# Performance work log

Measured on AMD Instinct MI355X. Metric: run time of the kernel, lower is better.

The kernel has to match this reference:

```python
import jax, jax.numpy as jnp
import numpy as np

HIDDEN = 1024
HEADS = 16
HEAD_DIM = HIDDEN // HEADS  # 64
MAX_SEQ = 2048


def _rope_tables():
    # RotaryEmbedding buffers: freqs_cos/sin of shape [max_seq_len, head_dim//2]
    inv_freq = 1.0 / (10000.0 ** (jnp.arange(0, HEAD_DIM, 2, dtype=jnp.float32) / HEAD_DIM))
    t = jnp.arange(MAX_SEQ, dtype=jnp.float32)
    freqs = t[:, None] * inv_freq[None, :]
    return jnp.cos(freqs), jnp.sin(freqs)


def setup_inputs() -> dict:
    key = jax.random.key(0)
    k1, k2, k3 = jax.random.split(key, 3)
    x = jax.random.normal(k1, (2, 2048, HIDDEN), dtype=jnp.float32)
    qkv_w = jax.random.normal(k2, (HIDDEN, 3 * HIDDEN), dtype=jnp.float32) * 0.02
    qkv_b = jnp.zeros((3 * HIDDEN,), dtype=jnp.float32)
    out_w = jax.random.normal(k3, (HIDDEN, HIDDEN), dtype=jnp.float32) * 0.02
    out_b = jnp.zeros((HIDDEN,), dtype=jnp.float32)
    return {"x": x, "qkv_w": qkv_w, "qkv_b": qkv_b, "out_w": out_w, "out_b": out_b}


def reference(x, qkv_w, qkv_b, out_w, out_b):
    b, s, _ = x.shape
    qkv = x @ qkv_w + qkv_b                                   # [b, s, 3*hidden]
    qkv = qkv.reshape(b, s, HEADS, 3 * HEAD_DIM).transpose(0, 2, 1, 3)  # [b, h, s, 3*hd]
    q, k, v = jnp.split(qkv, 3, axis=-1)                      # each [b, h, s, hd]

    # Faithful to source quirk: rotary() is called on [b, h, s, hd] tensors so
    # x.shape[1] == num_heads -> seq_pos = arange(num_heads); tables are indexed
    # by HEAD index and broadcast over the sequence axis.
    cos_tab, sin_tab = _rope_tables()
    cos = cos_tab[:HEADS][None, :, None, :]                   # [1, h, 1, hd/2]
    sin = sin_tab[:HEADS][None, :, None, :]

    def rot(u):
        u1 = u[..., : HEAD_DIM // 2]
        u2 = u[..., HEAD_DIM // 2 :]
        return jnp.concatenate([u1 * cos - u2 * sin, u2 * cos + u1 * sin], axis=-1)

    q = rot(q)
    k = rot(k)

    scores = jnp.einsum("bhqd,bhkd->bhqk", q, k) / (HEAD_DIM ** 0.5)  # [b, h, s, s]
    attn = jax.nn.softmax(scores.astype(jnp.float32), axis=-1).astype(scores.dtype)
    out = jnp.einsum("bhqk,bhkd->bhqd", attn, v)              # [b, h, s, hd]
    out = out.transpose(0, 2, 1, 3).reshape(b, s, HEADS * HEAD_DIM)
    return out @ out_w + out_b
```

## Files before the change

kernel.cpp:

```cpp
#include <hip/hip_runtime.h>
#include <hip/hip_bf16.h>
#include <cstdint>
#include <cstddef>

typedef float  f32x4  __attribute__((ext_vector_type(4)));
typedef __bf16 bf16x8 __attribute__((ext_vector_type(8)));
typedef __bf16 bf16x4 __attribute__((ext_vector_type(4)));

#define HIDDEN 1024
#define SEQ    2048
#define BATCH  2
#define NQKV   3072
#define MTOT   4096

__device__ __forceinline__ __bf16 f2bf(float f) {
  unsigned u = __builtin_bit_cast(unsigned, f);
  u += 0x7FFFu + ((u >> 16) & 1u);
  unsigned short s = (unsigned short)(u >> 16);
  return __builtin_bit_cast(__bf16, s);
}

__device__ __forceinline__ unsigned pk2(float a, float b) {
  unsigned ua = __builtin_bit_cast(unsigned, a) + 0x8000u;
  unsigned ub = __builtin_bit_cast(unsigned, b) + 0x8000u;
  return __builtin_amdgcn_perm(ub, ua, 0x07060302u);
}

__device__ __forceinline__ float fexp2(float x) {
#if __has_builtin(__builtin_amdgcn_exp2f)
  return __builtin_amdgcn_exp2f(x);
#else
  return exp2f(x);
#endif
}

__device__ __forceinline__ void async16(const void* g, void* l) {
  __builtin_amdgcn_global_load_lds((__attribute__((address_space(1))) void*)(g),
                                   (__attribute__((address_space(3))) void*)(l),
                                   16, 0, 0);
}

#define MFMA16(a, b, c) __builtin_amdgcn_mfma_f32_16x16x32_bf16((a), (b), (c), 0, 0, 0)

__global__ __launch_bounds__(256) void k_prep(const float* __restrict__ x,
                                              __bf16* __restrict__ xb,
                                              const float* __restrict__ qkv_w,
                                              __bf16* __restrict__ wqkT,
                                              const float* __restrict__ out_w,
                                              __bf16* __restrict__ woT) {
  __shared__ float tile[64][65];
  const int bid = blockIdx.x, t = threadIdx.x;
  if (bid < 4096) {
    int i = bid * 256 + t;
    float4 v = ((const float4*)x)[i];
    bf16x4 o;
    o[0] = f2bf(v.x); o[1] = f2bf(v.y); o[2] = f2bf(v.z); o[3] = f2bf(v.w);
    ((bf16x4*)xb)[i] = o;
    return;
  }
  const float* W; __bf16* WT; int N, bx, by;
  if (bid < 4864) { int g = bid - 4096; W = qkv_w; WT = wqkT; N = NQKV;  bx = g % 48; by = g / 48; }
  else            { int g = bid - 4864; W = out_w; WT = woT;  N = HIDDEN; bx = g % 16; by = g / 16; }
  const int K = HIDDEN;
  int tx = t & 63, ty = t >> 6;
  int n0 = bx * 64, k0 = by * 64;
#pragma unroll
  for (int r = 0; r < 16; r++) {
    int row = r * 4 + ty;
    tile[row][tx] = W[(size_t)(k0 + row) * N + n0 + tx];
  }
  __syncthreads();
#pragma unroll
  for (int i2 = 0; i2 < 2; i2++) {
    int cc = i2 * 256 + t;
    int n = cc >> 3, ch = cc & 7;
    bf16x8 o;
#pragma unroll
    for (int j = 0; j < 8; j++) o[j] = f2bf(tile[ch * 8 + j][n]);
    *(bf16x8*)(WT + (size_t)(n0 + n) * K + k0 + ch * 8) = o;
  }
}

__global__ __launch_bounds__(512, 2) void k_qkv(const __bf16* __restrict__ A,
                                                const __bf16* __restrict__ BT,
                                                const float* __restrict__ bias,
                                                __bf16* __restrict__ Cout,
                                                __bf16* __restrict__ vt) {
  const int K = HIDDEN;
  __shared__ __align__(16) __bf16 As[2][2][8192];
  __shared__ __align__(16) __bf16 Bs[2][12288];
  const int t = threadIdx.x;
  const int lane = t & 63, wv = t >> 6;
  const int ln = lane & 15, quad = lane >> 4;
  const int wm = (wv >> 2) * 128, wn = (wv & 3) * 48;

  const int lin = blockIdx.x;
  const int xcd = lin & 7, wi = lin >> 3;
  const int bxi = (xcd & 3) * 4 + (wi & 3);
  const int byi = (xcd >> 2) * 8 + (wi >> 2);
  const int m0 = byi * 256, n0 = bxi * 192;

  auto stA = [&](int kt, int h) {
    __bf16* dst = &As[kt & 1][h][0];
    const __bf16* src = A + (size_t)m0 * K + kt * 64;
#pragma unroll
    for (int i = 0; i < 2; i++) {
      int tt = i * 512 + t;
      int sr = tt >> 3, ch = tt & 7;
      int gr = (sr & 63) + ((sr >> 6) << 7) + h * 64;
      async16(src + (size_t)gr * K + ((ch ^ (sr & 7)) * 8), dst + tt * 8);
    }
  };
  auto stB = [&](int kt) {
    __bf16* dst = &Bs[kt & 1][0];
    const __bf16* src = BT + (size_t)n0 * K + kt * 64;
#pragma unroll
    for (int i = 0; i < 3; i++) {
      int tt = i * 512 + t;
      int row = tt >> 3, ch = tt & 7;
      async16(src + (size_t)row * K + ((ch ^ (row & 7)) * 8), dst + tt * 8);
    }
  };

  const f32x4 zero4 = {0.f, 0.f, 0.f, 0.f};
  f32x4 acc[8][3];
#pragma unroll
  for (int i = 0; i < 8; i++)
#pragma unroll
    for (int j = 0; j < 3; j++) acc[i][j] = zero4;

  stA(0, 0); stB(0); stA(0, 1); stA(1, 0); stB(1);

  bf16x8 a0[4], a1[4], b0[3], b1[3];
  const int sra = ln + ((wv >> 2) << 6);
  const int srb = (wv & 3) * 48 + ln;
  const int swz = ln & 7;

  const int NT = K / 64;
  for (int kt = 0; kt < NT; kt++) {
    const int p = kt & 1;
    if (kt < NT - 1) asm volatile("s_waitcnt vmcnt(5)" ::: "memory");
    else             asm volatile("s_waitcnt vmcnt(0)" ::: "memory");
    __builtin_amdgcn_s_barrier();
    const __bf16* A0 = &As[p][0][0];
    const __bf16* A1 = &As[p][1][0];
    const __bf16* Bb = &Bs[p][0];
    {
#pragma unroll
      for (int m = 0; m < 4; m++)
        a0[m] = *(const bf16x8*)(A0 + (sra + m * 16) * 64 + ((quad ^ swz) * 8));
#pragma unroll
      for (int n = 0; n < 3; n++)
        b0[n] = *(const bf16x8*)(Bb + (srb + n * 16) * 64 + ((quad ^ swz) * 8));
      if (kt + 1 < NT) stA(kt + 1, 1);
      __builtin_amdgcn_s_barrier();
      asm volatile("s_waitcnt lgkmcnt(0)" ::: "memory");
      __builtin_amdgcn_sched_barrier(0);
      __builtin_amdgcn_s_setprio(1);
#pragma unroll
      for (int m = 0; m < 4; m++)
#pragma unroll
        for (int n = 0; n < 3; n++)
          acc[m][n] = MFMA16(a0[m], b0[n], acc[m][n]);
      __builtin_amdgcn_s_setprio(0);
      __builtin_amdgcn_s_barrier();
    }
    {
#pragma unroll
      for (int m = 0; m < 4; m++)
        a1[m] = *(const bf16x8*)(A0 + (sra + m * 16) * 64 + (((4 + quad) ^ swz) * 8));
#pragma unroll
      for (int n = 0; n < 3; n++)
        b1[n] = *(const bf16x8*)(Bb + (srb + n * 16) * 64 + (((4 + quad) ^ swz) * 8));
      __builtin_amdgcn_s_barrier();
      asm volatile("s_waitcnt lgkmcnt(0)" ::: "memory");
      __builtin_amdgcn_sched_barrier(0);
      __builtin_amdgcn_s_setprio(1);
#pragma unroll
      for (int m = 0; m < 4; m++)
#pragma unroll
        for (int n = 0; n < 3; n++)
          acc[m][n] = MFMA16(a1[m], b1[n], acc[m][n]);
      __builtin_amdgcn_s_setprio(0);
      __builtin_amdgcn_s_barrier();
    }
    {
#pragma unroll
      for (int m = 0; m < 4; m++)
        a0[m] = *(const bf16x8*)(A1 + (sra + m * 16) * 64 + ((quad ^ swz) * 8));
      if (kt + 2 < NT) stA(kt + 2, 0);
      __builtin_amdgcn_s_barrier();
      asm volatile("s_waitcnt lgkmcnt(0)" ::: "memory");
      __builtin_amdgcn_sched_barrier(0);
      __builtin_amdgcn_s_setprio(1);
#pragma unroll
      for (int m = 0; m < 4; m++)
#pragma unroll
        for (int n = 0; n < 3; n++)
          acc[4 + m][n] = MFMA16(a0[m], b0[n], acc[4 + m][n]);
      __builtin_amdgcn_s_setprio(0);
      __builtin_amdgcn_s_barrier();
    }
    {
#pragma unroll
      for (int m = 0; m < 4; m++)
        a1[m] = *(const bf16x8*)(A1 + (sra + m * 16) * 64 + (((4 + quad) ^ swz) * 8));
      if (kt + 2 < NT) stB(kt + 2);
      __builtin_amdgcn_s_barrier();
      asm volatile("s_waitcnt lgkmcnt(0)" ::: "memory");
      __builtin_amdgcn_sched_barrier(0);
      __builtin_amdgcn_s_setprio(1);
#pragma unroll
      for (int m = 0; m < 4; m++)
#pragma unroll
        for (int n = 0; n < 3; n++)
          acc[4 + m][n] = MFMA16(a1[m], b1[n], acc[4 + m][n]);
      __builtin_amdgcn_s_setprio(0);
    }
  }

  const float CE = 0.125f * 1.44269504089f;
#pragma unroll
  for (int nt = 0; nt < 3; nt++) {
    int g = n0 + wn + nt * 16;
    int col = g + ln;
    float bv = bias[col];
    int off = g % 192;
    if (off < 128) {
      float scl = (off < 64) ? CE : 1.0f;
#pragma unroll
      for (int mt = 0; mt < 8; mt++) {
#pragma unroll
        for (int r = 0; r < 4; r++) {
          int row = m0 + wm + mt * 16 + quad * 4 + r;
          Cout[(size_t)row * NQKV + col] = f2bf((acc[mt][nt][r] + bv) * scl);
        }
      }
    } else {
      int hg = g / 192;
      int d  = off - 128 + ln;
#pragma unroll
      for (int mt = 0; mt < 8; mt++) {
        int rowb = m0 + wm + mt * 16;
        int bb = rowb >> 11;
        int s  = rowb & 2047;
        int sblk = s >> 7;
        int blk  = (s >> 4) & 7;
        int pp = (blk & 3) * 32 + quad * 8 + ((blk >> 2) << 2);
        uint2 o;
        o.x = pk2(acc[mt][nt][0] + bv, acc[mt][nt][1] + bv);
        o.y = pk2(acc[mt][nt][2] + bv, acc[mt][nt][3] + bv);
        *(uint2*)(vt + ((size_t)((bb * 16 + hg) * 64 + d)) * SEQ + sblk * 128 + pp) = o;
      }
    }
  }
}

__global__ __launch_bounds__(512, 2) void k_out(const __bf16* __restrict__ A,
                                                const __bf16* __restrict__ BT,
                                                const float* __restrict__ bias,
                                                float* __restrict__ Cout) {
  const int K = HIDDEN, N = HIDDEN;
  __shared__ __align__(16) __bf16 As[2][2][4096];
  __shared__ __align__(16) __bf16 Bs[2][8192];
  const int t = threadIdx.x;
  const int lane = t & 63, wv = t >> 6;
  const int ln = lane & 15, quad = lane >> 4;
  const int wm = (wv >> 2) * 64, wn = (wv & 3) * 32;

  const int lin = blockIdx.x;
  const int xcd = lin & 7, wi = lin >> 3;
  const int bxi = (xcd & 1) * 4 + (wi & 3);
  const int byi = (xcd >> 1) * 8 + (wi >> 2);
  const int m0 = byi * 128, n0 = bxi * 128;

  auto stA = [&](int kt, int h) {
    __bf16* dst = &As[kt & 1][h][0];
    const __bf16* src = A + (size_t)m0 * K + kt * 64;
    int sr = t >> 3, ch = t & 7;
    int gr = (sr & 31) + ((sr >> 5) << 6) + h * 32;
    async16(src + (size_t)gr * K + ((ch ^ (sr & 7)) * 8), dst + t * 8);
  };
  auto stB = [&](int kt) {
    __bf16* dst = &Bs[kt & 1][0];
    const __bf16* src = BT + (size_t)n0 * K + kt * 64;
#pragma unroll
    for (int i = 0; i < 2; i++) {
      int tt = i * 512 + t;
      int row = tt >> 3, ch = tt & 7;
      async16(src + (size_t)row * K + ((ch ^ (row & 7)) * 8), dst + tt * 8);
    }
  };

  const f32x4 zero4 = {0.f, 0.f, 0.f, 0.f};
  f32x4 acc[4][2];
#pragma unroll
  for (int i = 0; i < 4; i++)
#pragma unroll
    for (int j = 0; j < 2; j++) acc[i][j] = zero4;

  stA(0, 0); stB(0); stA(0, 1); stA(1, 0); stB(1);

  bf16x8 af[2][2], bfr[2][2];
  const int sra = ln + ((wv >> 2) << 5);
  const int srb = wn + ln;
  const int swz = ln & 7;

  const int NT = K / 64;
  for (int kt = 0; kt < NT; kt++) {
    const int p = kt & 1;
    if (kt < NT - 1) asm volatile("s_waitcnt vmcnt(3)" ::: "memory");
    else             asm volatile("s_waitcnt vmcnt(0)" ::: "memory");
    __builtin_amdgcn_s_barrier();
    const __bf16* A0 = &As[p][0][0];
    const __bf16* A1 = &As[p][1][0];
    const __bf16* Bb = &Bs[p][0];
    {
#pragma unroll
      for (int m = 0; m < 2; m++)
#pragma unroll
        for (int kk = 0; kk < 2; kk++)
          af[m][kk] = *(const bf16x8*)(A0 + (sra + m * 16) * 64 + (((kk * 4 + quad) ^ swz) * 8));
#pragma unroll
      for (int n = 0; n < 2; n++)
#pragma unroll
        for (int kk = 0; kk < 2; kk++)
          bfr[n][kk] = *(const bf16x8*)(Bb + (srb + n * 16) * 64 + (((kk * 4 + quad) ^ swz) * 8));
      if (kt + 1 < NT) stA(kt + 1, 1);
      __builtin_amdgcn_s_barrier();
      asm volatile("s_waitcnt lgkmcnt(0)" ::: "memory");
      __builtin_amdgcn_sched_barrier(0);
      __builtin_amdgcn_s_setprio(1);
#pragma unroll
      for (int m = 0; m < 2; m++)
#pragma unroll
        for (int n = 0; n < 2; n++) {
          acc[m][n] = MFMA16(af[m][0], bfr[n][0], acc[m][n]);
          acc[m][n] = MFMA16(af[m][1], bfr[n][1], acc[m][n]);
        }
      __builtin_amdgcn_s_setprio(0);
      __builtin_amdgcn_s_barrier();
    }
    {
#pragma unroll
      for (int m = 0; m < 2; m++)
#pragma unroll
        for (int kk = 0; kk < 2; kk++)
          af[m][kk] = *(const bf16x8*)(A1 + (sra + m * 16) * 64 + (((kk * 4 + quad) ^ swz) * 8));
      if (kt + 2 < NT) { stA(kt + 2, 0); stB(kt + 2); }
      __builtin_amdgcn_s_barrier();
      asm volatile("s_waitcnt lgkmcnt(0)" ::: "memory");
      __builtin_amdgcn_sched_barrier(0);
      __builtin_amdgcn_s_setprio(1);
#pragma unroll
      for (int m = 0; m < 2; m++)
#pragma unroll
        for (int n = 0; n < 2; n++) {
          acc[2 + m][n] = MFMA16(af[m][0], bfr[n][0], acc[2 + m][n]);
          acc[2 + m][n] = MFMA16(af[m][1], bfr[n][1], acc[2 + m][n]);
        }
      __builtin_amdgcn_s_setprio(0);
    }
  }

#pragma unroll
  for (int h = 0; h < 2; h++)
#pragma unroll
    for (int n = 0; n < 2; n++) {
      int col = n0 + wn + n * 16 + ln;
      float bv = bias[col];
#pragma unroll
      for (int m = 0; m < 2; m++)
#pragma unroll
        for (int r = 0; r < 4; r++) {
          int row = m0 + wm + h * 32 + m * 16 + quad * 4 + r;
          Cout[(size_t)row * N + col] = acc[h * 2 + m][n][r] + bv;
        }
    }
}

__global__ __launch_bounds__(512, 4) void k_attn(const __bf16* __restrict__ qkv,
                                                 const __bf16* __restrict__ vt,
                                                 __bf16* __restrict__ aout) {
  __shared__ __align__(16) __bf16 smem[32768];
  const int t = threadIdx.x;
  const int lane = t & 63, wv = t >> 6;
  const int ln = lane & 15, quad = lane >> 4;
  const int sw8 = (quad ^ ((ln >> 1) & 3)) * 8;

  int gid = blockIdx.x;
  int slot = gid & 7, j = gid >> 3;
  int bh = slot * 4 + (j >> 4);
  int qt0 = j & 15;
  const int b = bh >> 4, h = bh & 15;
  const int q0 = qt0 * 128;

  const __bf16* qbase = qkv + (size_t)b * SEQ * NQKV + h * 192;
  const __bf16* kbase = qbase + 64;
  const __bf16* vbase = vt + (size_t)bh * 64 * SEQ;

#pragma unroll
  for (int i = 0; i < 2; i++) {
    int tt = i * 512 + t;
    int hh = tt >> 9, row = (tt >> 2) & 127, ch = tt & 3;
    int chs = ch ^ ((row >> 1) & 3);
    async16(kbase + (size_t)row * NQKV + hh * 32 + chs * 8, smem + tt * 8);
  }
#pragma unroll
  for (int i = 0; i < 2; i++) {
    int tt = i * 512 + t;
    int c = tt >> 8, d = (tt >> 2) & 63, w = tt & 3;
    int ws = w ^ ((d >> 1) & 3);
    async16(vbase + (size_t)d * SEQ + c * 32 + ws * 8, smem + 16384 + tt * 8);
  }

  bf16x8 qf[2];
#pragma unroll
  for (int dc = 0; dc < 2; dc++)
    qf[dc] = *(const bf16x8*)(qbase + (size_t)(q0 + wv * 16 + ln) * NQKV + dc * 32 + quad * 8);

  union { unsigned u[4]; bf16x8 v; } ones;
  ones.u[0] = ones.u[1] = ones.u[2] = ones.u[3] = 0x3F803F80u;

  const f32x4 zero4 = {0.f, 0.f, 0.f, 0.f};
  f32x4 O[4];
  f32x4 Ol = zero4;
#pragma unroll
  for (int dt = 0; dt < 4; dt++) O[dt] = zero4;

  for (int it = 0; it < SEQ / 128; it++) {
    __syncthreads();
    const __bf16* Ks = smem + (it & 1) * 8192;
    const __bf16* Vs = smem + 16384 + (it & 1) * 8192;
    if (it + 1 < SEQ / 128) {
      __bf16* Kd = smem + ((it + 1) & 1) * 8192;
      __bf16* Vd = smem + 16384 + ((it + 1) & 1) * 8192;
      const __bf16* kn = kbase + (size_t)(it + 1) * 128 * NQKV;
      const __bf16* vn = vbase + (it + 1) * 128;
#pragma unroll
      for (int i = 0; i < 2; i++) {
        int tt = i * 512 + t;
        int hh = tt >> 9, row = (tt >> 2) & 127, ch = tt & 3;
        int chs = ch ^ ((row >> 1) & 3);
        async16(kn + (size_t)row * NQKV + hh * 32 + chs * 8, Kd + tt * 8);
      }
#pragma unroll
      for (int i = 0; i < 2; i++) {
        int tt = i * 512 + t;
        int c = tt >> 8, d = (tt >> 2) & 63, w = tt & 3;
        int ws = w ^ ((d >> 1) & 3);
        async16(vn + (size_t)d * SEQ + c * 32 + ws * 8, Vd + tt * 8);
      }
    }

    unsigned Pp[8][2];
#pragma unroll
    for (int blk = 0; blk < 8; blk++) {
      bf16x8 kf0 = *(const bf16x8*)(Ks +        (blk * 16 + ln) * 32 + sw8);
      bf16x8 kf1 = *(const bf16x8*)(Ks + 4096 + (blk * 16 + ln) * 32 + sw8);
      __builtin_amdgcn_s_setprio(1);
      f32x4 s = MFMA16(kf0, qf[0], zero4);
      s = MFMA16(kf1, qf[1], s);
      __builtin_amdgcn_s_setprio(0);
      Pp[blk][0] = pk2(fexp2(s[0]), fexp2(s[1]));
      Pp[blk][1] = pk2(fexp2(s[2]), fexp2(s[3]));
    }
#pragma unroll
    for (int kc = 0; kc < 4; kc++) {
      union { bf16x8 v; unsigned u[4]; } pf;
      pf.u[0] = Pp[kc][0]; pf.u[1] = Pp[kc][1];
      pf.u[2] = Pp[kc + 4][0]; pf.u[3] = Pp[kc + 4][1];
      __builtin_amdgcn_s_setprio(1);
      Ol = MFMA16(pf.v, ones.v, Ol);
#pragma unroll
      for (int dt = 0; dt < 4; dt++) {
        bf16x8 vf = *(const bf16x8*)(Vs + kc * 2048 + (dt * 16 + ln) * 32 + sw8);
        O[dt] = MFMA16(pf.v, vf, O[dt]);
      }
      __builtin_amdgcn_s_setprio(0);
    }
  }

  __bf16* stage = smem + wv * 1024;
#pragma unroll
  for (int r = 0; r < 4; r++) {
    float ir = 1.0f / Ol[r];
#pragma unroll
    for (int dt = 0; dt < 4; dt++)
      stage[(quad * 4 + r) * 64 + dt * 16 + ln] = f2bf(O[dt][r] * ir);
  }
  __bf16* obase = aout + (size_t)(b * SEQ + q0 + wv * 16) * HIDDEN + h * 64;
#pragma unroll
  for (int i = 0; i < 2; i++) {
    int tt = i * 64 + lane; int row = tt >> 3, ch = tt & 7;
    *(bf16x8*)(obase + (size_t)row * HIDDEN + ch * 8) = *(const bf16x8*)(stage + row * 64 + ch * 8);
  }
}

extern "C" void kernel_launch(void* const* d_in, const int* in_sizes, int n_in,
                              void* d_out, int out_size, void* d_ws, size_t ws_size,
                              hipStream_t stream) {
  const float* x     = (const float*)d_in[0];
  const float* qkv_w = (const float*)d_in[1];
  const float* qkv_b = (const float*)d_in[2];
  const float* out_w = (const float*)d_in[3];
  const float* out_b = (const float*)d_in[4];

  char* ws = (char*)d_ws;
  __bf16* xb   = (__bf16*)(ws);
  __bf16* wqkT = (__bf16*)(ws + 8388608);
  __bf16* woT  = (__bf16*)(ws + 14680064);
  __bf16* qkv  = (__bf16*)(ws + 16777216);
  __bf16* vt   = (__bf16*)(ws + 41943040);
  __bf16* aout = (__bf16*)(ws + 50331648);

  k_prep<<<5120, 256, 0, stream>>>(x, xb, qkv_w, wqkT, out_w, woT);
  k_qkv<<<256, 512, 0, stream>>>(xb, wqkT, qkv_b, qkv, vt);
  k_attn<<<512, 512, 0, stream>>>(qkv, vt, aout);
  k_out<<<256, 512, 0, stream>>>(aout, woT, out_b, (float*)d_out);
}
```

Before: 172.4 us.

## Process two query tiles per attention block to reuse K/V tiles

Each attention block now handles 256 query rows instead of 128: every wave keeps two Q fragments and two sets of output accumulators. Each K/V tile loaded into shared memory feeds twice as many MFMAs, and the grid is halved. This cuts K/V global traffic and LDS reads per unit of work, in exchange for more registers (launch bounds lowered to 2), lower occupancy and fewer blocks (256) to spread across the CUs.

```diff
diff --git a/kernel.cpp b/kernel.cpp
--- a/kernel.cpp
+++ b/kernel.cpp
@@ -379,7 +379,7 @@
     }
 }
 
-__global__ __launch_bounds__(512, 4) void k_attn(const __bf16* __restrict__ qkv,
+__global__ __launch_bounds__(512, 2) void k_attn(const __bf16* __restrict__ qkv,
                                                  const __bf16* __restrict__ vt,
                                                  __bf16* __restrict__ aout) {
   __shared__ __align__(16) __bf16 smem[32768];
@@ -390,10 +390,10 @@
 
   int gid = blockIdx.x;
   int slot = gid & 7, j = gid >> 3;
-  int bh = slot * 4 + (j >> 4);
-  int qt0 = j & 15;
+  int bh = slot * 4 + (j >> 3);
+  int qt0 = j & 7;
   const int b = bh >> 4, h = bh & 15;
-  const int q0 = qt0 * 128;
+  const int q0 = qt0 * 256;
 
   const __bf16* qbase = qkv + (size_t)b * SEQ * NQKV + h * 192;
   const __bf16* kbase = qbase + 64;
@@ -414,19 +414,24 @@
     async16(vbase + (size_t)d * SEQ + c * 32 + ws * 8, smem + 16384 + tt * 8);
   }
 
-  bf16x8 qf[2];
-#pragma unroll
-  for (int dc = 0; dc < 2; dc++)
-    qf[dc] = *(const bf16x8*)(qbase + (size_t)(q0 + wv * 16 + ln) * NQKV + dc * 32 + quad * 8);
+  bf16x8 qf[2][2];
+#pragma unroll
+  for (int u = 0; u < 2; u++)
+#pragma unroll
+    for (int dc = 0; dc < 2; dc++)
+      qf[u][dc] = *(const bf16x8*)(qbase + (size_t)(q0 + u * 128 + wv * 16 + ln) * NQKV + dc * 32 + quad * 8);
 
   union { unsigned u[4]; bf16x8 v; } ones;
   ones.u[0] = ones.u[1] = ones.u[2] = ones.u[3] = 0x3F803F80u;
 
   const f32x4 zero4 = {0.f, 0.f, 0.f, 0.f};
-  f32x4 O[4];
-  f32x4 Ol = zero4;
-#pragma unroll
-  for (int dt = 0; dt < 4; dt++) O[dt] = zero4;
+  f32x4 O[2][4];
+  f32x4 Ol[2];
+  Ol[0] = zero4; Ol[1] = zero4;
+#pragma unroll
+  for (int u = 0; u < 2; u++)
+#pragma unroll
+    for (int dt = 0; dt < 4; dt++) O[u][dt] = zero4;
 
   for (int it = 0; it < SEQ / 128; it++) {
     __syncthreads();
@@ -453,47 +458,61 @@
       }
     }
 
-    unsigned Pp[8][2];
+    unsigned Pp[2][8][2];
 #pragma unroll
     for (int blk = 0; blk < 8; blk++) {
       bf16x8 kf0 = *(const bf16x8*)(Ks +        (blk * 16 + ln) * 32 + sw8);
       bf16x8 kf1 = *(const bf16x8*)(Ks + 4096 + (blk * 16 + ln) * 32 + sw8);
       __builtin_amdgcn_s_setprio(1);
-      f32x4 s = MFMA16(kf0, qf[0], zero4);
-      s = MFMA16(kf1, qf[1], s);
-      __builtin_amdgcn_s_setprio(0);
-      Pp[blk][0] = pk2(fexp2(s[0]), fexp2(s[1]));
-      Pp[blk][1] = pk2(fexp2(s[2]), fexp2(s[3]));
+      f32x4 s0 = MFMA16(kf0, qf[0][0], zero4);
+      f32x4 s1 = MFMA16(kf0, qf[1][0], zero4);
+      s0 = MFMA16(kf1, qf[0][1], s0);
+      s1 = MFMA16(kf1, qf[1][1], s1);
+      __builtin_amdgcn_s_setprio(0);
+      Pp[0][blk][0] = pk2(fexp2(s0[0]), fexp2(s0[1]));
+      Pp[0][blk][1] = pk2(fexp2(s0[2]), fexp2(s0[3]));
+      Pp[1][blk][0] = pk2(fexp2(s1[0]), fexp2(s1[1]));
+      Pp[1][blk][1] = pk2(fexp2(s1[2]), fexp2(s1[3]));
     }
 #pragma unroll
     for (int kc = 0; kc < 4; kc++) {
-      union { bf16x8 v; unsigned u[4]; } pf;
-      pf.u[0] = Pp[kc][0]; pf.u[1] = Pp[kc][1];
-      pf.u[2] = Pp[kc + 4][0]; pf.u[3] = Pp[kc + 4][1];
-      __builtin_amdgcn_s_setprio(1);
-      Ol = MFMA16(pf.v, ones.v, Ol);
+      union { bf16x8 v; unsigned u[4]; } pf0, pf1;
+      pf0.u[0] = Pp[0][kc][0]; pf0.u[1] = Pp[0][kc][1];
+      pf0.u[2] = Pp[0][kc + 4][0]; pf0.u[3] = Pp[0][kc + 4][1];
+      pf1.u[0] = Pp[1][kc][0]; pf1.u[1] = Pp[1][kc][1];
+      pf1.u[2] = Pp[1][kc + 4][0]; pf1.u[3] = Pp[1][kc + 4][1];
+      __builtin_amdgcn_s_setprio(1);
+      Ol[0] = MFMA16(pf0.v, ones.v, Ol[0]);
+      Ol[1] = MFMA16(pf1.v, ones.v, Ol[1]);
 #pragma unroll
       for (int dt = 0; dt < 4; dt++) {
         bf16x8 vf = *(const bf16x8*)(Vs + kc * 2048 + (dt * 16 + ln) * 32 + sw8);
-        O[dt] = MFMA16(pf.v, vf, O[dt]);
+        O[0][dt] = MFMA16(pf0.v, vf, O[0][dt]);
+        O[1][dt] = MFMA16(pf1.v, vf, O[1][dt]);
       }
       __builtin_amdgcn_s_setprio(0);
     }
   }
 
-  __bf16* stage = smem + wv * 1024;
-#pragma unroll
-  for (int r = 0; r < 4; r++) {
-    float ir = 1.0f / Ol[r];
-#pragma unroll
-    for (int dt = 0; dt < 4; dt++)
-      stage[(quad * 4 + r) * 64 + dt * 16 + ln] = f2bf(O[dt][r] * ir);
-  }
-  __bf16* obase = aout + (size_t)(b * SEQ + q0 + wv * 16) * HIDDEN + h * 64;
-#pragma unroll
-  for (int i = 0; i < 2; i++) {
-    int tt = i * 64 + lane; int row = tt >> 3, ch = tt & 7;
-    *(bf16x8*)(obase + (size_t)row * HIDDEN + ch * 8) = *(const bf16x8*)(stage + row * 64 + ch * 8);
+  __bf16* stage = smem + (wv & 3) * 2048 + (wv >> 2) * 16384;
+#pragma unroll
+  for (int u = 0; u < 2; u++)
+#pragma unroll
+    for (int r = 0; r < 4; r++) {
+      float ir = 1.0f / Ol[u][r];
+#pragma unroll
+      for (int dt = 0; dt < 4; dt++)
+        stage[u * 1024 + (quad * 4 + r) * 64 + dt * 16 + ln] = f2bf(O[u][dt][r] * ir);
+    }
+#pragma unroll
+  for (int u = 0; u < 2; u++) {
+    __bf16* obase = aout + (size_t)(b * SEQ + q0 + u * 128 + wv * 16) * HIDDEN + h * 64;
+#pragma unroll
+    for (int i = 0; i < 2; i++) {
+      int tt = i * 64 + lane; int row = tt >> 3, ch = tt & 7;
+      *(bf16x8*)(obase + (size_t)row * HIDDEN + ch * 8) =
+          *(const bf16x8*)(stage + u * 1024 + row * 64 + ch * 8);
+    }
   }
 }
 
@@ -516,6 +535,6 @@
 
   k_prep<<<5120, 256, 0, stream>>>(x, xb, qkv_w, wqkT, out_w, woT);
   k_qkv<<<256, 512, 0, stream>>>(xb, wqkT, qkv_b, qkv, vt);
-  k_attn<<<512, 512, 0, stream>>>(qkv, vt, aout);
+  k_attn<<<256, 512, 0, stream>>>(qkv, vt, aout);
   k_out<<<256, 512, 0, stream>>>(aout, woT, out_b, (float*)d_out);
 }
```

Result: no change. 173.2 us (+0.5%).

## Software-pipeline attention loop: overlap next QK^T with current PV

Applied to the files above, without the earlier changes.

Restructures the attention main loop into a two-stage software pipeline. The QK^T and exp for tile it+1 are computed while the PV product for tile it runs, using two register P buffers and a manually unrolled even/odd loop. K is prefetched two tiles ahead and V one tile ahead. The goal is to interleave the exp/VALU work with MFMA and hide shared-memory load latency, at the cost of more registers (a second P buffer) and different sync placement.

```diff
diff --git a/kernel.cpp b/kernel.cpp
--- a/kernel.cpp
+++ b/kernel.cpp
@@ -399,20 +399,30 @@
   const __bf16* kbase = qbase + 64;
   const __bf16* vbase = vt + (size_t)bh * 64 * SEQ;
 
-#pragma unroll
-  for (int i = 0; i < 2; i++) {
-    int tt = i * 512 + t;
-    int hh = tt >> 9, row = (tt >> 2) & 127, ch = tt & 3;
-    int chs = ch ^ ((row >> 1) & 3);
-    async16(kbase + (size_t)row * NQKV + hh * 32 + chs * 8, smem + tt * 8);
-  }
-#pragma unroll
-  for (int i = 0; i < 2; i++) {
-    int tt = i * 512 + t;
-    int c = tt >> 8, d = (tt >> 2) & 63, w = tt & 3;
-    int ws = w ^ ((d >> 1) & 3);
-    async16(vbase + (size_t)d * SEQ + c * 32 + ws * 8, smem + 16384 + tt * 8);
-  }
+  auto stageK = [&](int it) {
+    __bf16* Kd = smem + (it & 1) * 8192;
+    const __bf16* kn = kbase + (size_t)it * 128 * NQKV;
+#pragma unroll
+    for (int i = 0; i < 2; i++) {
+      int tt = i * 512 + t;
+      int hh = tt >> 9, row = (tt >> 2) & 127, ch = tt & 3;
+      int chs = ch ^ ((row >> 1) & 3);
+      async16(kn + (size_t)row * NQKV + hh * 32 + chs * 8, Kd + tt * 8);
+    }
+  };
+  auto stageV = [&](int it) {
+    __bf16* Vd = smem + 16384 + (it & 1) * 8192;
+    const __bf16* vn = vbase + it * 128;
+#pragma unroll
+    for (int i = 0; i < 2; i++) {
+      int tt = i * 512 + t;
+      int c = tt >> 8, d = (tt >> 2) & 63, w = tt & 3;
+      int ws = w ^ ((d >> 1) & 3);
+      async16(vn + (size_t)d * SEQ + c * 32 + ws * 8, Vd + tt * 8);
+    }
+  };
+
+  stageK(0); stageV(0); stageK(1);
 
   bf16x8 qf[2];
 #pragma unroll
@@ -428,32 +438,9 @@
 #pragma unroll
   for (int dt = 0; dt < 4; dt++) O[dt] = zero4;
 
-  for (int it = 0; it < SEQ / 128; it++) {
-    __syncthreads();
-    const __bf16* Ks = smem + (it & 1) * 8192;
-    const __bf16* Vs = smem + 16384 + (it & 1) * 8192;
-    if (it + 1 < SEQ / 128) {
-      __bf16* Kd = smem + ((it + 1) & 1) * 8192;
-      __bf16* Vd = smem + 16384 + ((it + 1) & 1) * 8192;
-      const __bf16* kn = kbase + (size_t)(it + 1) * 128 * NQKV;
-      const __bf16* vn = vbase + (it + 1) * 128;
-#pragma unroll
-      for (int i = 0; i < 2; i++) {
-        int tt = i * 512 + t;
-        int hh = tt >> 9, row = (tt >> 2) & 127, ch = tt & 3;
-        int chs = ch ^ ((row >> 1) & 3);
-        async16(kn + (size_t)row * NQKV + hh * 32 + chs * 8, Kd + tt * 8);
-      }
-#pragma unroll
-      for (int i = 0; i < 2; i++) {
-        int tt = i * 512 + t;
-        int c = tt >> 8, d = (tt >> 2) & 63, w = tt & 3;
-        int ws = w ^ ((d >> 1) & 3);
-        async16(vn + (size_t)d * SEQ + c * 32 + ws * 8, Vd + tt * 8);
-      }
-    }
-
-    unsigned Pp[8][2];
+  unsigned Pa[8][2], Pb[8][2];
+
+  auto qkt = [&](const __bf16* Ks, unsigned (&P)[8][2]) {
 #pragma unroll
     for (int blk = 0; blk < 8; blk++) {
       bf16x8 kf0 = *(const bf16x8*)(Ks +        (blk * 16 + ln) * 32 + sw8);
@@ -462,14 +449,16 @@
       f32x4 s = MFMA16(kf0, qf[0], zero4);
       s = MFMA16(kf1, qf[1], s);
       __builtin_amdgcn_s_setprio(0);
-      Pp[blk][0] = pk2(fexp2(s[0]), fexp2(s[1]));
-      Pp[blk][1] = pk2(fexp2(s[2]), fexp2(s[3]));
-    }
+      P[blk][0] = pk2(fexp2(s[0]), fexp2(s[1]));
+      P[blk][1] = pk2(fexp2(s[2]), fexp2(s[3]));
+    }
+  };
+  auto pv = [&](const __bf16* Vs, unsigned (&P)[8][2]) {
 #pragma unroll
     for (int kc = 0; kc < 4; kc++) {
       union { bf16x8 v; unsigned u[4]; } pf;
-      pf.u[0] = Pp[kc][0]; pf.u[1] = Pp[kc][1];
-      pf.u[2] = Pp[kc + 4][0]; pf.u[3] = Pp[kc + 4][1];
+      pf.u[0] = P[kc][0]; pf.u[1] = P[kc][1];
+      pf.u[2] = P[kc + 4][0]; pf.u[3] = P[kc + 4][1];
       __builtin_amdgcn_s_setprio(1);
       Ol = MFMA16(pf.v, ones.v, Ol);
 #pragma unroll
@@ -479,6 +468,23 @@
       }
       __builtin_amdgcn_s_setprio(0);
     }
+  };
+
+  __syncthreads();
+  qkt(smem, Pa);
+
+  for (int itp = 0; itp < 8; itp++) {
+    const int itE = 2 * itp, itO = 2 * itp + 1;
+    __syncthreads();
+    if (itE + 2 < 16) stageK(itE + 2);
+    stageV(itE + 1);
+    qkt(smem + 8192, Pb);
+    pv(smem + 16384, Pa);
+    __syncthreads();
+    if (itO + 2 < 16) stageK(itO + 2);
+    if (itO + 1 < 16) stageV(itO + 1);
+    if (itO < 15) qkt(smem, Pa);
+    pv(smem + 16384 + 8192, Pb);
   }
 
   __bf16* stage = smem + wv * 1024;
```

Result: no change. 174.7 us (+1.4%).
